# Kernel optimization log

Hardware: AMD Instinct MI355X
Metric: run time of the kernel (lower is better)

## Reference

```python
import jax, jax.numpy as jnp
import numpy as np

T, B, C, H, W = 4, 8, 256, 16, 16
HEADS = 8
N = H * W
TN = T * N
DH = C // HEADS
DECAY = 0.25

# STE quantizer: fwd round(clamp(x,0,1)); bwd passes grad only where 0<=x<=1
@jax.custom_vjp
def quant1(x):
    return jnp.round(jnp.clip(x, 0.0, 1.0))

def _q_fwd(x):
    return quant1(x), x

def _q_bwd(x, g):
    return (jnp.where((x < 0) | (x > 1), 0.0, g),)

quant1.defvjp(_q_fwd, _q_bwd)

def lif(x):
    # x: [T, ...]; sequential LIF membrane decay + quantize over leading (time) axis
    def step(carry, xt):
        mem_old, spike = carry
        mem = (mem_old - jax.lax.stop_gradient(spike) * 0.5) * DECAY + xt
        s = quant1(mem)
        return (mem, s), s
    z = jnp.zeros_like(x[0])
    _, out = jax.lax.scan(step, (z, z), x)
    return out

def bn1d(x, gamma, beta, mean, var):
    # eval-mode BatchNorm1d over channel axis 1 of [B, Ch, L]
    inv = jax.lax.rsqrt(var + 1e-5)
    return (x - mean[None, :, None]) * (gamma * inv)[None, :, None] + beta[None, :, None]

def _rel_pos_index():
    coords = np.stack(np.meshgrid(np.arange(T), np.arange(H), np.arange(W), indexing='ij'))  # [3,T,H,W]
    cf = coords.reshape(3, -1)                      # [3, TN]
    rc = (cf[:, :, None] - cf[:, None, :]).transpose(1, 2, 0).copy()  # [TN, TN, 3]
    rc[:, :, 0] += T - 1
    rc[:, :, 1] += H - 1
    rc[:, :, 2] += W - 1
    rc[:, :, 0] *= (2 * H - 1) * (2 * W - 1)
    rc[:, :, 1] *= (2 * W - 1)
    return rc.sum(-1)                               # [TN, TN] ints

def _mask():
    m = np.ones((TN, TN), np.float32)
    for t in range(T - 1):
        m[t * N:(t + 1) * N, (t + 1) * N:] = 0.0
    return m

_RPI = jnp.asarray(_rel_pos_index().reshape(-1))
_MASK = jnp.asarray(_mask())


def setup_inputs() -> dict:
    key = jax.random.key(0)
    ks = jax.random.split(key, 13)
    bias_rows = (2 * T - 1) * (2 * H - 1) * (2 * W - 1)
    return {
        'x': jax.random.normal(ks[0], (T, B, C, H, W), jnp.float32),
        'w_qkv': jax.random.normal(ks[1], (3 * C, C), jnp.float32) * 0.05,
        'qkv_gamma': jax.random.uniform(ks[2], (3 * C,), jnp.float32, 0.5, 1.5),
        'qkv_beta': jax.random.normal(ks[3], (3 * C,), jnp.float32) * 0.1,
        'qkv_mean': jax.random.normal(ks[4], (3 * C,), jnp.float32) * 0.1,
        'qkv_var': jax.random.uniform(ks[5], (3 * C,), jnp.float32, 0.5, 1.5),
        'bias_table': jax.random.normal(ks[6], (bias_rows, HEADS), jnp.float32) * 0.02,
        'w_proj': jax.random.normal(ks[7], (C, C), jnp.float32) * 0.05,
        'b_proj': jax.random.normal(ks[8], (C,), jnp.float32) * 0.02,
        'proj_gamma': jax.random.uniform(ks[9], (C,), jnp.float32, 0.5, 1.5),
        'proj_beta': jax.random.normal(ks[10], (C,), jnp.float32) * 0.1,
        'proj_mean': jax.random.normal(ks[11], (C,), jnp.float32) * 0.1,
        'proj_var': jax.random.uniform(ks[12], (C,), jnp.float32, 0.5, 1.5),
    }


def reference(x, w_qkv, qkv_gamma, qkv_beta, qkv_mean, qkv_var, bias_table,
              w_proj, b_proj, proj_gamma, proj_beta, proj_mean, proj_var):
    # flatten spatial, then raw reshape [T,B,C,N] -> [B,C,T*N] (as in torch source)
    xf = x.reshape(T, B, C, N).reshape(B, C, T * N)
    # 1x1 conv == channel matmul, then eval BN
    qkv = jnp.einsum('oc,bcl->bol', w_qkv, xf)
    qkv = bn1d(qkv, qkv_gamma, qkv_beta, qkv_mean, qkv_var)
    qkv = qkv.reshape(B, 3 * C, T, N).transpose(2, 0, 1, 3)  # [T,B,3C,N]
    qkv = lif(qkv).transpose(1, 0, 3, 2)                      # [B,T,N,3C]
    q, k, v = jnp.split(qkv, 3, axis=-1)                      # each [B,T,N,C]

    def to_heads(z):  # b t n (h d) -> b h (t n) d
        return z.reshape(B, T, N, HEADS, DH).transpose(0, 3, 1, 2, 4).reshape(B, HEADS, TN, DH)
    q, k, v = map(to_heads, (q, k, v))

    bias = bias_table[_RPI].reshape(TN, TN, HEADS).transpose(2, 0, 1)  # [h,TN,TN]
    attn = jnp.einsum('bhnd,bhmd->bhnm', q, k) + bias[None]
    attn = attn * _MASK[None, None]                                     # block upper-triangle mask
    o = jnp.einsum('bhnm,bhmd->bhnd', attn, v) * 0.125                  # [B,h,TN,d]

    o = o.transpose(0, 2, 1, 3).reshape(B, TN, C).reshape(B, T, N, C).transpose(1, 0, 3, 2)  # [T,B,C,N]
    o = lif(o)
    o = o.transpose(1, 2, 0, 3).reshape(B, C, T * N)          # [B,C,TN]
    o = jnp.einsum('oc,bcl->bol', w_proj, o) + b_proj[None, :, None]
    o = bn1d(o, proj_gamma, proj_beta, proj_mean, proj_var)
    o = o.reshape(B, C, T, N).transpose(2, 0, 1, 3).reshape(T, B, C, H, W)
    return lif(o)
```

## Files before the change

kernel.cpp:

```cpp
#include <hip/hip_runtime.h>
#include <stdint.h>
#include <math.h>

constexpr int T_ = 4;
constexpr int B_ = 8;
constexpr int C_ = 256;
constexpr int N_ = 256;
constexpr int TN_ = 1024;
constexpr int NH_ = 8;
constexpr int O3_ = 768;
constexpr int BIAS_ROWS_ = 6727;

__device__ __constant__ int TI_OF[10] = {0,1,1,2,2,2,3,3,3,3};
__device__ __constant__ int TJ_OF[10] = {0,0,1,0,1,2,0,1,2,3};

__device__ __forceinline__ float quant1f(float m) {
    return rintf(fminf(fmaxf(m, 0.0f), 1.0f));
}

__global__ __launch_bounds__(256) void k1_qkv_gemm(
    const float* __restrict__ x, const float* __restrict__ w,
    const float* __restrict__ gamma, const float* __restrict__ beta,
    const float* __restrict__ mean, const float* __restrict__ var,
    float* __restrict__ out)
{
    __shared__ float At[16][68];
    __shared__ float Bt[16][132];
    const int b = blockIdx.z;
    const int oBase = blockIdx.y * 64;
    const int lBase = blockIdx.x * 128;
    const int tid = threadIdx.x;
    const int tx = tid & 31;
    const int ty = tid >> 5;
    const float* xb = x + (size_t)b * C_ * TN_;

    float acc[8][4];
#pragma unroll
    for (int i = 0; i < 8; ++i)
#pragma unroll
        for (int j = 0; j < 4; ++j) acc[i][j] = 0.0f;

    const int b_kk = tid >> 4, b_c4 = (tid & 15) * 4;
    const int a_row = tid >> 3, a_k2 = (tid & 7) * 2;

    for (int kc = 0; kc < 16; ++kc) {
        const int k0 = kc * 16;
#pragma unroll
        for (int r = 0; r < 2; ++r) {
            const int row = a_row + 32 * r;
            const float2 v = *(const float2*)&w[(size_t)(oBase + row) * C_ + k0 + a_k2];
            At[a_k2][row] = v.x;
            At[a_k2 + 1][row] = v.y;
        }
#pragma unroll
        for (int r = 0; r < 2; ++r) {
            const float4 v = *(const float4*)&xb[(size_t)(k0 + b_kk) * TN_ + lBase + b_c4 + 64 * r];
            *(float4*)&Bt[b_kk][b_c4 + 64 * r] = v;
        }
        __syncthreads();
#pragma unroll
        for (int cc = 0; cc < 16; ++cc) {
            float a[8], bb[4];
            *(float4*)&a[0] = *(const float4*)&At[cc][ty * 4];
            *(float4*)&a[4] = *(const float4*)&At[cc][32 + ty * 4];
            *(float4*)&bb[0] = *(const float4*)&Bt[cc][tx * 4];
#pragma unroll
            for (int i = 0; i < 8; ++i)
#pragma unroll
                for (int j = 0; j < 4; ++j) acc[i][j] += a[i] * bb[j];
        }
        __syncthreads();
    }

#pragma unroll
    for (int i = 0; i < 8; ++i) {
        const int o = oBase + (i >> 2) * 32 + ty * 4 + (i & 3);
        const float inv = 1.0f / sqrtf(var[o] + 1e-5f);
        const float g = gamma[o] * inv;
        const float mn = mean[o], bt = beta[o];
        float4 st;
        st.x = (acc[i][0] - mn) * g + bt;
        st.y = (acc[i][1] - mn) * g + bt;
        st.z = (acc[i][2] - mn) * g + bt;
        st.w = (acc[i][3] - mn) * g + bt;
        *(float4*)&out[((size_t)b * O3_ + o) * TN_ + lBase + tx * 4] = st;
    }
}

__global__ __launch_bounds__(256) void k2_lif_pack(
    const float* __restrict__ qkv,
    uint32_t* __restrict__ qb, uint32_t* __restrict__ kb, uint32_t* __restrict__ vb)
{
    const int n = threadIdx.x;
    const int g = blockIdx.x;
    const int b = blockIdx.y;
    const int which = g >> 3, h = g & 7;
    uint32_t* dst = (which == 0) ? qb : (which == 1) ? kb : vb;
    const float* src = qkv + ((size_t)b * O3_ + g * 32) * TN_;

    float memv[32];
#pragma unroll
    for (int d = 0; d < 32; ++d) memv[d] = 0.0f;
    uint32_t prev = 0;

    for (int t = 0; t < T_; ++t) {
        uint32_t bits = 0;
#pragma unroll
        for (int d = 0; d < 32; ++d) {
            const float xv = src[(size_t)d * TN_ + t * N_ + n];
            const float m = (memv[d] - 0.5f * (float)((prev >> d) & 1u)) * 0.25f + xv;
            memv[d] = m;
            const float s = quant1f(m);
            bits |= ((uint32_t)s) << d;
        }
        prev = bits;
        dst[((size_t)b * NH_ + h) * TN_ + t * N_ + n] = bits;
    }
}

__global__ __launch_bounds__(256) void k3_tg(
    const uint32_t* __restrict__ kb, const uint32_t* __restrict__ vb,
    float* __restrict__ Gf)
{
    __shared__ uint64_t ks[4][32][4];
    __shared__ uint64_t vs[4][32][4];
    const int bh = blockIdx.x;
    const int tid = threadIdx.x;
    const int q = tid >> 6, lane = tid & 63;

#pragma unroll
    for (int t = 0; t < T_; ++t) {
        const int j = t * N_ + q * 64 + lane;
        const uint32_t kw = kb[(size_t)bh * TN_ + j];
        const uint32_t vw = vb[(size_t)bh * TN_ + j];
#pragma unroll
        for (int d = 0; d < 32; ++d) {
            const uint64_t mk = __ballot((kw >> d) & 1u);
            const uint64_t mv = __ballot((vw >> d) & 1u);
            if (lane == 0) { ks[t][d][q] = mk; vs[t][d][q] = mv; }
        }
    }
    __syncthreads();

    const int d = tid & 31;
#pragma unroll
    for (int s = 0; s < 4; ++s) {
        const int d2 = (tid >> 5) + 8 * s;
        int cum = 0;
#pragma unroll
        for (int t = 0; t < T_; ++t) {
            int p = 0;
#pragma unroll
            for (int w = 0; w < 4; ++w) p += __popcll(ks[t][d2][w] & vs[t][d][w]);
            cum += p;
            Gf[(size_t)(bh * 4 + t) * 1024 + d2 * 32 + d] = (float)cum;
        }
    }
}

__global__ __launch_bounds__(256) void k3_s1(
    const uint32_t* __restrict__ qb, const float* __restrict__ Gf,
    float* __restrict__ oatt)
{
    const int grp = blockIdx.x;
    const int ti = grp >> 2, seg = grp & 3;
    const int h = blockIdx.y;
    const int b = blockIdx.z;
    const int bh = b * NH_ + h;
    const int tid = threadIdx.x;
    const int d = tid & 31;
    const int ig = tid >> 5;

    const float* gsrc = Gf + (size_t)(bh * 4 + ti) * 1024 + d;
    float g[32];
#pragma unroll
    for (int d2 = 0; d2 < 32; ++d2) g[d2] = gsrc[d2 * 32];

    const uint32_t* qbh = qb + (size_t)bh * TN_;
    const int i0 = ti * N_ + seg * 64 + ig * 8;
#pragma unroll
    for (int s = 0; s < 8; ++s) {
        const int i = i0 + s;
        const uint32_t q = qbh[i];
        float acc = 0.0f;
#pragma unroll
        for (int d2 = 0; d2 < 32; ++d2)
            acc += ((q >> d2) & 1u) ? g[d2] : 0.0f;
        oatt[((size_t)b * TN_ + i) * C_ + h * 32 + d] = acc;
    }
}

__global__ __launch_bounds__(256) void k3_bias_gemm(
    const uint32_t* __restrict__ vb, const float* __restrict__ bias_table,
    float* __restrict__ p0, float* __restrict__ p1,
    float* __restrict__ p2, float* __restrict__ p3)
{
    __shared__ float sbl[640];
    __shared__ float At[16][68];
    __shared__ float Bt[16][132];

    const int z = blockIdx.z;
    const int h = z / 10;
    const int p = z % 10;
    const int ti = TI_OF[p], tj = TJ_OF[p];
    const int dt = ti - tj;
    const int iT = blockIdx.y;
    const int nBase = blockIdx.x * 128;
    const int tid = threadIdx.x;

    const int base = 3363 + 961 * dt + 124 * iT - 480;
    for (int s = tid; s < 640; s += 256) {
        const int gidx = base + s;
        sbl[s] = (gidx < BIAS_ROWS_) ? bias_table[(size_t)gidx * NH_ + h] : 0.0f;
    }

    const int ty = tid >> 4, tx = tid & 15;

    const int ccS = tx;
    const int iBase4 = ty * 4;
    const int sIdxBase = 31 * (iBase4 >> 4) + (iBase4 & 15) + 480 - ccS;

    const int kkS = ty;
    const int n8 = tx * 8;
    const int nS = nBase + n8;
    const int bS = nS >> 5, d0S = nS & 31;
    const uint32_t* vbw = vb + ((size_t)bS * NH_ + h) * TN_ + tj * 256 + kkS;

    float acc[4][8];
#pragma unroll
    for (int i = 0; i < 4; ++i)
#pragma unroll
        for (int j = 0; j < 8; ++j) acc[i][j] = 0.0f;

    __syncthreads();

    for (int kc = 0; kc < 16; ++kc) {
        {
            const int s0 = sIdxBase - 31 * kc;
            float4 av;
            av.x = sbl[s0];
            av.y = sbl[s0 + 1];
            av.z = sbl[s0 + 2];
            av.w = sbl[s0 + 3];
            *(float4*)&At[ccS][iBase4] = av;
        }
        {
            const uint32_t wd = vbw[kc * 16];
            float4 b0, b1;
            b0.x = (float)((wd >> d0S) & 1u);
            b0.y = (float)((wd >> (d0S + 1)) & 1u);
            b0.z = (float)((wd >> (d0S + 2)) & 1u);
            b0.w = (float)((wd >> (d0S + 3)) & 1u);
            b1.x = (float)((wd >> (d0S + 4)) & 1u);
            b1.y = (float)((wd >> (d0S + 5)) & 1u);
            b1.z = (float)((wd >> (d0S + 6)) & 1u);
            b1.w = (float)((wd >> (d0S + 7)) & 1u);
            *(float4*)&Bt[kkS][n8] = b0;
            *(float4*)&Bt[kkS][n8 + 4] = b1;
        }
        __syncthreads();
#pragma unroll
        for (int cc = 0; cc < 16; ++cc) {
            float a[4], bb[8];
            *(float4*)&a[0] = *(const float4*)&At[cc][ty * 4];
            *(float4*)&bb[0] = *(const float4*)&Bt[cc][tx * 8];
            *(float4*)&bb[4] = *(const float4*)&Bt[cc][tx * 8 + 4];
#pragma unroll
            for (int i = 0; i < 4; ++i)
#pragma unroll
                for (int j = 0; j < 8; ++j) acc[i][j] += a[i] * bb[j];
        }
        __syncthreads();
    }

    float* plane = (tj == 0) ? p0 : (tj == 1) ? p1 : (tj == 2) ? p2 : p3;
    const int nrows = (4 - tj) * 256;
    const int c0 = h * 32 + d0S;
#pragma unroll
    for (int r = 0; r < 4; ++r) {
        const int rowL = dt * 256 + iT * 64 + ty * 4 + r;
        float* dst = &plane[((size_t)bS * nrows + rowL) * 256 + c0];
        float4 s0, s1;
        s0.x = acc[r][0]; s0.y = acc[r][1]; s0.z = acc[r][2]; s0.w = acc[r][3];
        s1.x = acc[r][4]; s1.y = acc[r][5]; s1.z = acc[r][6]; s1.w = acc[r][7];
        *(float4*)&dst[0] = s0;
        *(float4*)&dst[4] = s1;
    }
}

__global__ __launch_bounds__(256) void k4_lif2(
    const float* __restrict__ oatt,
    const float* __restrict__ p0, const float* __restrict__ p1,
    const float* __restrict__ p2, const float* __restrict__ p3,
    uint32_t* __restrict__ s2c)
{
    const int c = threadIdx.x;
    const int n = blockIdx.x;
    const int b = blockIdx.y;
    const int lane = c & 63;
    float memv = 0.0f, spk = 0.0f;
    for (int t = 0; t < T_; ++t) {
        const int l = t * N_ + n;
        float v = oatt[((size_t)b * TN_ + l) * C_ + c];
        v += p0[((size_t)b * 1024 + l) * 256 + c];
        if (t >= 1) v += p1[((size_t)b * 768 + (l - 256)) * 256 + c];
        if (t >= 2) v += p2[((size_t)b * 512 + (l - 512)) * 256 + c];
        if (t >= 3) v += p3[((size_t)b * 256 + (l - 768)) * 256 + c];
        const float m = (memv - 0.5f * spk) * 0.25f + 0.125f * v;
        memv = m;
        const float s = quant1f(m);
        spk = s;
        const uint64_t mask = __ballot(s != 0.0f);
        if (lane == 0)
            s2c[((size_t)b * TN_ + l) * 8 + (c >> 5)] = (uint32_t)mask;
        else if (lane == 32)
            s2c[((size_t)b * TN_ + l) * 8 + (c >> 5)] = (uint32_t)(mask >> 32);
    }
}

__global__ __launch_bounds__(256) void k5_proj_gemm(
    const uint32_t* __restrict__ s2c, const float* __restrict__ w,
    const float* __restrict__ bp,
    const float* __restrict__ gamma, const float* __restrict__ beta,
    const float* __restrict__ mean, const float* __restrict__ var,
    float* __restrict__ pbn)
{
    __shared__ float At[16][36];
    __shared__ float Bt[16][132];
    const int b = blockIdx.z;
    const int oBase = blockIdx.y * 32;
    const int lBase = blockIdx.x * 128;
    const int tid = threadIdx.x;
    const int tx = tid & 31;
    const int ty = tid >> 5;

    const int a_row = tid >> 3, a_k2 = (tid & 7) * 2;
    const int b_ll = tid >> 1, b_sub = tid & 1;
    const uint32_t* srow = s2c + ((size_t)b * TN_ + lBase + b_ll) * 8;

    float acc[4][4];
#pragma unroll
    for (int i = 0; i < 4; ++i)
#pragma unroll
        for (int j = 0; j < 4; ++j) acc[i][j] = 0.0f;

    for (int kc = 0; kc < 16; ++kc) {
        const int k0 = kc * 16;
        {
            const float2 v = *(const float2*)&w[(size_t)(oBase + a_row) * C_ + k0 + a_k2];
            At[a_k2][a_row] = v.x;
            At[a_k2 + 1][a_row] = v.y;
        }
        {
            const uint32_t wd = srow[kc >> 1];
            const int sh = ((kc & 1) << 4) + (b_sub << 3);
#pragma unroll
            for (int u = 0; u < 8; ++u)
                Bt[(b_sub << 3) + u][b_ll] = (float)((wd >> (sh + u)) & 1u);
        }
        __syncthreads();
#pragma unroll
        for (int cc = 0; cc < 16; ++cc) {
            float a[4], bb[4];
            *(float4*)&a[0] = *(const float4*)&At[cc][ty * 4];
            *(float4*)&bb[0] = *(const float4*)&Bt[cc][tx * 4];
#pragma unroll
            for (int i = 0; i < 4; ++i)
#pragma unroll
                for (int j = 0; j < 4; ++j) acc[i][j] += a[i] * bb[j];
        }
        __syncthreads();
    }

#pragma unroll
    for (int i = 0; i < 4; ++i) {
        const int o = oBase + ty * 4 + i;
        const float inv = 1.0f / sqrtf(var[o] + 1e-5f);
        const float g = gamma[o] * inv;
        const float mn = mean[o], bt = beta[o], bpo = bp[o];
        float4 st;
        st.x = ((acc[i][0] + bpo) - mn) * g + bt;
        st.y = ((acc[i][1] + bpo) - mn) * g + bt;
        st.z = ((acc[i][2] + bpo) - mn) * g + bt;
        st.w = ((acc[i][3] + bpo) - mn) * g + bt;
        *(float4*)&pbn[((size_t)b * C_ + o) * TN_ + lBase + tx * 4] = st;
    }
}

__global__ __launch_bounds__(256) void k6_lif3(
    const float* __restrict__ pbn, float* __restrict__ out)
{
    const int n = threadIdx.x;
    const int c = blockIdx.x;
    const int b = blockIdx.y;
    const float* src = pbn + ((size_t)b * C_ + c) * TN_;
    float memv = 0.0f, spk = 0.0f;
    for (int t = 0; t < T_; ++t) {
        const float m = (memv - 0.5f * spk) * 0.25f + src[t * N_ + n];
        memv = m;
        const float s = quant1f(m);
        out[(((size_t)t * B_ + b) * C_ + c) * N_ + n] = s;
        spk = s;
    }
}

extern "C" void kernel_launch(void* const* d_in, const int* in_sizes, int n_in,
                              void* d_out, int out_size, void* d_ws, size_t ws_size,
                              hipStream_t stream)
{
    const float* x          = (const float*)d_in[0];
    const float* w_qkv      = (const float*)d_in[1];
    const float* qkv_gamma  = (const float*)d_in[2];
    const float* qkv_beta   = (const float*)d_in[3];
    const float* qkv_mean   = (const float*)d_in[4];
    const float* qkv_var    = (const float*)d_in[5];
    const float* bias_table = (const float*)d_in[6];
    const float* w_proj     = (const float*)d_in[7];
    const float* b_proj     = (const float*)d_in[8];
    const float* proj_gamma = (const float*)d_in[9];
    const float* proj_beta  = (const float*)d_in[10];
    const float* proj_mean  = (const float*)d_in[11];
    const float* proj_var   = (const float*)d_in[12];
    float* out = (float*)d_out;

    char* ws = (char*)d_ws;
    float*    qkv_bn = (float*)(ws + 0);
    float*    Gf     = (float*)(ws + 524288);
    float*    part0  = (float*)(ws + 1048576);
    float*    part1  = (float*)(ws + 9437184);
    float*    part2  = (float*)(ws + 15728640);
    float*    part3  = (float*)(ws + 19922944);
    float*    oatt   = (float*)(ws + 25165824);
    uint32_t* s2c    = (uint32_t*)(ws + 33554432);
    float*    pbn    = (float*)(ws + 41943040);
    uint32_t* qbits  = (uint32_t*)(ws + 50331648);
    uint32_t* kbits  = (uint32_t*)(ws + 50593792);
    uint32_t* vbits  = (uint32_t*)(ws + 50855936);

    k1_qkv_gemm<<<dim3(8, 12, 8), 256, 0, stream>>>(
        x, w_qkv, qkv_gamma, qkv_beta, qkv_mean, qkv_var, qkv_bn);

    k2_lif_pack<<<dim3(24, 8), 256, 0, stream>>>(qkv_bn, qbits, kbits, vbits);

    k3_tg<<<dim3(64), 256, 0, stream>>>(kbits, vbits, Gf);

    k3_s1<<<dim3(16, 8, 8), 256, 0, stream>>>(qbits, Gf, oatt);

    k3_bias_gemm<<<dim3(2, 4, 80), 256, 0, stream>>>(
        vbits, bias_table, part0, part1, part2, part3);

    k4_lif2<<<dim3(256, 8), 256, 0, stream>>>(oatt, part0, part1, part2, part3, s2c);

    k5_proj_gemm<<<dim3(8, 8, 8), 256, 0, stream>>>(
        s2c, w_proj, b_proj, proj_gamma, proj_beta, proj_mean, proj_var, pbn);

    k6_lif3<<<dim3(256, 8), 256, 0, stream>>>(pbn, out);
}
```

Before: 229.8 us.

## Fuse proj GEMM with final LIF, enlarge QKV GEMM tiles, split LIF pack threads

The projection GEMM now tiles over (t, n) so each thread holds all four timesteps of one output element. This lets it apply the final LIF in registers and write spikes directly, which removes the pbn round trip and the separate LIF kernel. The QKV GEMM tile grows to 96x256 with a 12x8 per-thread micro-tile and launch_bounds(256,1), trading occupancy for more reuse. The LIF pack kernel splits the 32 channel bits across two threads merged with a shuffle, doubling parallelism.

```diff
diff --git a/kernel.cpp b/kernel.cpp
--- a/kernel.cpp
+++ b/kernel.cpp
@@ -18,72 +18,80 @@
     return rintf(fminf(fmaxf(m, 0.0f), 1.0f));
 }
 
-__global__ __launch_bounds__(256) void k1_qkv_gemm(
+__global__ __launch_bounds__(256, 1) void k1_qkv_gemm(
     const float* __restrict__ x, const float* __restrict__ w,
     const float* __restrict__ gamma, const float* __restrict__ beta,
     const float* __restrict__ mean, const float* __restrict__ var,
     float* __restrict__ out)
 {
-    __shared__ float At[16][68];
-    __shared__ float Bt[16][132];
+    __shared__ float At[16][100];
+    __shared__ float Bt[16][264];
     const int b = blockIdx.z;
-    const int oBase = blockIdx.y * 64;
-    const int lBase = blockIdx.x * 128;
+    const int oBase = blockIdx.y * 96;
+    const int lBase = blockIdx.x * 256;
     const int tid = threadIdx.x;
     const int tx = tid & 31;
     const int ty = tid >> 5;
     const float* xb = x + (size_t)b * C_ * TN_;
 
-    float acc[8][4];
-#pragma unroll
-    for (int i = 0; i < 8; ++i)
-#pragma unroll
-        for (int j = 0; j < 4; ++j) acc[i][j] = 0.0f;
-
-    const int b_kk = tid >> 4, b_c4 = (tid & 15) * 4;
+    float acc[12][8];
+#pragma unroll
+    for (int i = 0; i < 12; ++i)
+#pragma unroll
+        for (int j = 0; j < 8; ++j) acc[i][j] = 0.0f;
+
     const int a_row = tid >> 3, a_k2 = (tid & 7) * 2;
+    const int b_kk = tid >> 4, b_c16 = (tid & 15) * 16;
 
     for (int kc = 0; kc < 16; ++kc) {
         const int k0 = kc * 16;
 #pragma unroll
-        for (int r = 0; r < 2; ++r) {
+        for (int r = 0; r < 3; ++r) {
             const int row = a_row + 32 * r;
             const float2 v = *(const float2*)&w[(size_t)(oBase + row) * C_ + k0 + a_k2];
             At[a_k2][row] = v.x;
             At[a_k2 + 1][row] = v.y;
         }
 #pragma unroll
-        for (int r = 0; r < 2; ++r) {
-            const float4 v = *(const float4*)&xb[(size_t)(k0 + b_kk) * TN_ + lBase + b_c4 + 64 * r];
-            *(float4*)&Bt[b_kk][b_c4 + 64 * r] = v;
+        for (int r = 0; r < 4; ++r) {
+            const float4 v = *(const float4*)&xb[(size_t)(k0 + b_kk) * TN_ + lBase + b_c16 + 4 * r];
+            *(float4*)&Bt[b_kk][b_c16 + 4 * r] = v;
         }
         __syncthreads();
 #pragma unroll
         for (int cc = 0; cc < 16; ++cc) {
-            float a[8], bb[4];
+            float a[12], bb[8];
             *(float4*)&a[0] = *(const float4*)&At[cc][ty * 4];
             *(float4*)&a[4] = *(const float4*)&At[cc][32 + ty * 4];
-            *(float4*)&bb[0] = *(const float4*)&Bt[cc][tx * 4];
-#pragma unroll
-            for (int i = 0; i < 8; ++i)
-#pragma unroll
-                for (int j = 0; j < 4; ++j) acc[i][j] += a[i] * bb[j];
+            *(float4*)&a[8] = *(const float4*)&At[cc][64 + ty * 4];
+            *(float4*)&bb[0] = *(const float4*)&Bt[cc][tx * 8];
+            *(float4*)&bb[4] = *(const float4*)&Bt[cc][tx * 8 + 4];
+#pragma unroll
+            for (int i = 0; i < 12; ++i)
+#pragma unroll
+                for (int j = 0; j < 8; ++j) acc[i][j] += a[i] * bb[j];
         }
         __syncthreads();
     }
 
 #pragma unroll
-    for (int i = 0; i < 8; ++i) {
+    for (int i = 0; i < 12; ++i) {
         const int o = oBase + (i >> 2) * 32 + ty * 4 + (i & 3);
         const float inv = 1.0f / sqrtf(var[o] + 1e-5f);
         const float g = gamma[o] * inv;
         const float mn = mean[o], bt = beta[o];
-        float4 st;
-        st.x = (acc[i][0] - mn) * g + bt;
-        st.y = (acc[i][1] - mn) * g + bt;
-        st.z = (acc[i][2] - mn) * g + bt;
-        st.w = (acc[i][3] - mn) * g + bt;
-        *(float4*)&out[((size_t)b * O3_ + o) * TN_ + lBase + tx * 4] = st;
+        float4 s0, s1;
+        s0.x = (acc[i][0] - mn) * g + bt;
+        s0.y = (acc[i][1] - mn) * g + bt;
+        s0.z = (acc[i][2] - mn) * g + bt;
+        s0.w = (acc[i][3] - mn) * g + bt;
+        s1.x = (acc[i][4] - mn) * g + bt;
+        s1.y = (acc[i][5] - mn) * g + bt;
+        s1.z = (acc[i][6] - mn) * g + bt;
+        s1.w = (acc[i][7] - mn) * g + bt;
+        float* dst = &out[((size_t)b * O3_ + o) * TN_ + lBase + tx * 8];
+        *(float4*)&dst[0] = s0;
+        *(float4*)&dst[4] = s1;
     }
 }
 
@@ -91,30 +99,35 @@
     const float* __restrict__ qkv,
     uint32_t* __restrict__ qb, uint32_t* __restrict__ kb, uint32_t* __restrict__ vb)
 {
-    const int n = threadIdx.x;
+    const int tid = threadIdx.x;
     const int g = blockIdx.x;
     const int b = blockIdx.y;
+    const int n = blockIdx.z * 128 + (tid >> 1);
+    const int dh = tid & 1;
+    const int dbase = dh * 16;
     const int which = g >> 3, h = g & 7;
     uint32_t* dst = (which == 0) ? qb : (which == 1) ? kb : vb;
-    const float* src = qkv + ((size_t)b * O3_ + g * 32) * TN_;
-
-    float memv[32];
-#pragma unroll
-    for (int d = 0; d < 32; ++d) memv[d] = 0.0f;
-    uint32_t prev = 0;
+    const float* src = qkv + ((size_t)b * O3_ + g * 32 + dbase) * TN_;
+
+    float memv[16];
+#pragma unroll
+    for (int d = 0; d < 16; ++d) memv[d] = 0.0f;
+    uint32_t prevFull = 0;
 
     for (int t = 0; t < T_; ++t) {
         uint32_t bits = 0;
 #pragma unroll
-        for (int d = 0; d < 32; ++d) {
-            const float xv = src[(size_t)d * TN_ + t * N_ + n];
-            const float m = (memv[d] - 0.5f * (float)((prev >> d) & 1u)) * 0.25f + xv;
-            memv[d] = m;
+        for (int dd = 0; dd < 16; ++dd) {
+            const float xv = src[(size_t)dd * TN_ + t * N_ + n];
+            const float m = (memv[dd] - 0.5f * (float)((prevFull >> (dbase + dd)) & 1u)) * 0.25f + xv;
+            memv[dd] = m;
             const float s = quant1f(m);
-            bits |= ((uint32_t)s) << d;
-        }
-        prev = bits;
-        dst[((size_t)b * NH_ + h) * TN_ + t * N_ + n] = bits;
+            bits |= ((uint32_t)s) << (dbase + dd);
+        }
+        const uint32_t full = bits | (uint32_t)__shfl_xor((int)bits, 1);
+        prevFull = full;
+        if (dh == 0)
+            dst[((size_t)b * NH_ + h) * TN_ + t * N_ + n] = full;
     }
 }
 
@@ -318,89 +331,86 @@
     }
 }
 
-__global__ __launch_bounds__(256) void k5_proj_gemm(
+__global__ __launch_bounds__(256) void k5_proj_lif(
     const uint32_t* __restrict__ s2c, const float* __restrict__ w,
     const float* __restrict__ bp,
     const float* __restrict__ gamma, const float* __restrict__ beta,
     const float* __restrict__ mean, const float* __restrict__ var,
-    float* __restrict__ pbn)
-{
-    __shared__ float At[16][36];
-    __shared__ float Bt[16][132];
+    float* __restrict__ out)
+{
+    __shared__ float At[128][36];
+    __shared__ uint32_t Sw[128 * 9];
+    const int nBase = blockIdx.x * 32;
+    const int oBase = blockIdx.y * 32;
     const int b = blockIdx.z;
-    const int oBase = blockIdx.y * 32;
-    const int lBase = blockIdx.x * 128;
     const int tid = threadIdx.x;
     const int tx = tid & 31;
     const int ty = tid >> 5;
 
-    const int a_row = tid >> 3, a_k2 = (tid & 7) * 2;
-    const int b_ll = tid >> 1, b_sub = tid & 1;
-    const uint32_t* srow = s2c + ((size_t)b * TN_ + lBase + b_ll) * 8;
+#pragma unroll
+    for (int j = 0; j < 4; ++j) {
+        const int fidx = tid * 4 + j;
+        const int lp = fidx >> 3, wsel = fidx & 7;
+        const int t = lp >> 5, nn = lp & 31;
+        Sw[lp * 9 + wsel] = s2c[((size_t)b * TN_ + t * 256 + nBase + nn) * 8 + wsel];
+    }
+
+    const int a_row = tid >> 3, a_kq = (tid & 7) * 16;
 
     float acc[4][4];
 #pragma unroll
-    for (int i = 0; i < 4; ++i)
-#pragma unroll
-        for (int j = 0; j < 4; ++j) acc[i][j] = 0.0f;
-
-    for (int kc = 0; kc < 16; ++kc) {
-        const int k0 = kc * 16;
-        {
-            const float2 v = *(const float2*)&w[(size_t)(oBase + a_row) * C_ + k0 + a_k2];
-            At[a_k2][a_row] = v.x;
-            At[a_k2 + 1][a_row] = v.y;
-        }
-        {
-            const uint32_t wd = srow[kc >> 1];
-            const int sh = ((kc & 1) << 4) + (b_sub << 3);
-#pragma unroll
-            for (int u = 0; u < 8; ++u)
-                Bt[(b_sub << 3) + u][b_ll] = (float)((wd >> (sh + u)) & 1u);
+    for (int r = 0; r < 4; ++r)
+#pragma unroll
+        for (int t = 0; t < 4; ++t) acc[r][t] = 0.0f;
+
+    for (int half = 0; half < 2; ++half) {
+        if (half) __syncthreads();
+#pragma unroll
+        for (int j = 0; j < 4; ++j) {
+            const float4 v = *(const float4*)&w[(size_t)(oBase + a_row) * C_ + half * 128 + a_kq + 4 * j];
+            At[a_kq + 4 * j][a_row] = v.x;
+            At[a_kq + 4 * j + 1][a_row] = v.y;
+            At[a_kq + 4 * j + 2][a_row] = v.z;
+            At[a_kq + 4 * j + 3][a_row] = v.w;
         }
         __syncthreads();
-#pragma unroll
-        for (int cc = 0; cc < 16; ++cc) {
-            float a[4], bb[4];
-            *(float4*)&a[0] = *(const float4*)&At[cc][ty * 4];
-            *(float4*)&bb[0] = *(const float4*)&Bt[cc][tx * 4];
-#pragma unroll
-            for (int i = 0; i < 4; ++i)
-#pragma unroll
-                for (int j = 0; j < 4; ++j) acc[i][j] += a[i] * bb[j];
-        }
-        __syncthreads();
-    }
-
-#pragma unroll
-    for (int i = 0; i < 4; ++i) {
-        const int o = oBase + ty * 4 + i;
+
+        for (int ks = 0; ks < 4; ++ks) {
+            uint32_t wr[4];
+#pragma unroll
+            for (int t = 0; t < 4; ++t)
+                wr[t] = Sw[(t * 32 + tx) * 9 + half * 4 + ks];
+#pragma unroll
+            for (int u = 0; u < 32; ++u) {
+                float a[4];
+                *(float4*)&a[0] = *(const float4*)&At[ks * 32 + u][ty * 4];
+                float bv[4];
+#pragma unroll
+                for (int t = 0; t < 4; ++t) bv[t] = (float)((wr[t] >> u) & 1u);
+#pragma unroll
+                for (int r = 0; r < 4; ++r)
+#pragma unroll
+                    for (int t = 0; t < 4; ++t) acc[r][t] += a[r] * bv[t];
+            }
+        }
+    }
+
+#pragma unroll
+    for (int r = 0; r < 4; ++r) {
+        const int o = oBase + ty * 4 + r;
         const float inv = 1.0f / sqrtf(var[o] + 1e-5f);
         const float g = gamma[o] * inv;
         const float mn = mean[o], bt = beta[o], bpo = bp[o];
-        float4 st;
-        st.x = ((acc[i][0] + bpo) - mn) * g + bt;
-        st.y = ((acc[i][1] + bpo) - mn) * g + bt;
-        st.z = ((acc[i][2] + bpo) - mn) * g + bt;
-        st.w = ((acc[i][3] + bpo) - mn) * g + bt;
-        *(float4*)&pbn[((size_t)b * C_ + o) * TN_ + lBase + tx * 4] = st;
-    }
-}
-
-__global__ __launch_bounds__(256) void k6_lif3(
-    const float* __restrict__ pbn, float* __restrict__ out)
-{
-    const int n = threadIdx.x;
-    const int c = blockIdx.x;
-    const int b = blockIdx.y;
-    const float* src = pbn + ((size_t)b * C_ + c) * TN_;
-    float memv = 0.0f, spk = 0.0f;
-    for (int t = 0; t < T_; ++t) {
-        const float m = (memv - 0.5f * spk) * 0.25f + src[t * N_ + n];
-        memv = m;
-        const float s = quant1f(m);
-        out[(((size_t)t * B_ + b) * C_ + c) * N_ + n] = s;
-        spk = s;
+        float memv = 0.0f, spk = 0.0f;
+#pragma unroll
+        for (int t = 0; t < 4; ++t) {
+            const float val = ((acc[r][t] + bpo) - mn) * g + bt;
+            const float m = (memv - 0.5f * spk) * 0.25f + val;
+            memv = m;
+            const float s = quant1f(m);
+            spk = s;
+            out[(((size_t)t * B_ + b) * C_ + o) * N_ + nBase + tx] = s;
+        }
     }
 }
 
@@ -432,15 +442,14 @@
     float*    part3  = (float*)(ws + 19922944);
     float*    oatt   = (float*)(ws + 25165824);
     uint32_t* s2c    = (uint32_t*)(ws + 33554432);
-    float*    pbn    = (float*)(ws + 41943040);
     uint32_t* qbits  = (uint32_t*)(ws + 50331648);
     uint32_t* kbits  = (uint32_t*)(ws + 50593792);
     uint32_t* vbits  = (uint32_t*)(ws + 50855936);
 
-    k1_qkv_gemm<<<dim3(8, 12, 8), 256, 0, stream>>>(
+    k1_qkv_gemm<<<dim3(4, 8, 8), 256, 0, stream>>>(
         x, w_qkv, qkv_gamma, qkv_beta, qkv_mean, qkv_var, qkv_bn);
 
-    k2_lif_pack<<<dim3(24, 8), 256, 0, stream>>>(qkv_bn, qbits, kbits, vbits);
+    k2_lif_pack<<<dim3(24, 8, 2), 256, 0, stream>>>(qkv_bn, qbits, kbits, vbits);
 
     k3_tg<<<dim3(64), 256, 0, stream>>>(kbits, vbits, Gf);
 
@@ -451,8 +460,6 @@
 
     k4_lif2<<<dim3(256, 8), 256, 0, stream>>>(oatt, part0, part1, part2, part3, s2c);
 
-    k5_proj_gemm<<<dim3(8, 8, 8), 256, 0, stream>>>(
-        s2c, w_proj, b_proj, proj_gamma, proj_beta, proj_mean, proj_var, pbn);
-
-    k6_lif3<<<dim3(256, 8), 256, 0, stream>>>(pbn, out);
-}
+    k5_proj_lif<<<dim3(8, 8, 8), 256, 0, stream>>>(
+        s2c, w_proj, b_proj, proj_gamma, proj_beta, proj_mean, proj_var, out);
+}
```

Result: slower. 250.9 us (+9.2%).
